# Optimization experiments

Measured on AMD Instinct MI355X. Metric: run time of the kernel, lower is better.

## Reference

```python
import jax, jax.numpy as jnp
import numpy as np

K = 4096       # in_features (reduction dim)
N = 11008      # out_features
GROUP = 128    # scale group size along K
PACK = 8       # int4 values per int32


def dequantize_int4(packed, scales):
    """packed: [K//8, N] int32 (8 int4 nibbles per word along K),
    scales: [K//GROUP, N] fp16. Returns fp16 weight [K, N] with
    w = (nibble - 8) * scale (symmetric zero-point-8 scheme)."""
    shifts = (jnp.arange(PACK, dtype=jnp.int32) * 4)
    # [K//8, 8, N] -> [K, N]
    nibbles = (packed[:, None, :] >> shifts[None, :, None]) & 0xF
    q = nibbles.reshape(K, N)
    s = jnp.repeat(scales, GROUP, axis=0)  # [K, N]
    return (q.astype(jnp.float16) - jnp.float16(8.0)) * s


def setup_inputs() -> dict:
    key = jax.random.key(0)
    k1, k2, k3, k4 = jax.random.split(key, 4)
    x = jax.random.normal(k1, (4, 1024, K), dtype=jnp.float16)
    packed = jax.random.randint(k2, (K // PACK, N), 0, 2147483647, dtype=jnp.int32)
    scales = (jax.random.uniform(k3, (K // GROUP, N), dtype=jnp.float32) * 0.02 + 0.001).astype(jnp.float16)
    bias = jax.random.normal(k4, (N,), dtype=jnp.float16)
    return {"x": x, "packed": packed, "scales": scales, "bias": bias}


def reference(x, packed, scales, bias):
    in_shape = x.shape
    x2 = x.reshape(-1, in_shape[-1]).astype(jnp.float16)  # [M, K]
    w = dequantize_int4(packed, scales)                    # [K, N]
    out = jnp.matmul(x2, w)                                # [M, N] fp16
    out = out.reshape(*in_shape[:-1], -1)
    return out + bias
```

## Files before the change

kernel.cpp:

```cpp
#include <hip/hip_runtime.h>
#include <hip/hip_bf16.h>
#include <stdint.h>

#define K_DIM 4096
#define N_DIM 11008
#define BM 256
#define BN 128
#define NT (K_DIM / 64)

typedef _Float16 half8 __attribute__((ext_vector_type(8)));
typedef _Float16 half2v __attribute__((ext_vector_type(2)));
typedef float floatx4 __attribute__((ext_vector_type(4)));

typedef const uint32_t __attribute__((address_space(1)))* gas_u32p;
typedef uint32_t __attribute__((address_space(3)))* las_u32p;

__device__ __forceinline__ void glds16(const void* g, void* l) {
    __builtin_amdgcn_global_load_lds((gas_u32p)g, (las_u32p)l, 16, 0, 0);
}

__device__ __forceinline__ half8 dequant_word_pk(uint32_t w, half2v s2) {
    const uint32_t M = 0x000F000Fu;
    const uint32_t B = 0x64006400u;
    union { uint32_t u; half2v h; } t0, t1, t2, t3;
    t0.u = (w & M) | B;
    t1.u = ((w >> 4) & M) | B;
    t2.u = ((w >> 8) & M) | B;
    t3.u = ((w >> 12) & M) | B;
    const half2v off = {(_Float16)1032.0f, (_Float16)1032.0f};
    union { half8 h8; half2v h2[4]; } o;
    o.h2[0] = (t0.h - off) * s2;
    o.h2[1] = (t1.h - off) * s2;
    o.h2[2] = (t2.h - off) * s2;
    o.h2[3] = (t3.h - off) * s2;
    return o.h8;
}

__device__ __forceinline__ half8 dequant_word_f16(uint32_t w, float s) {
    half8 r;
    #pragma unroll
    for (int j = 0; j < 8; ++j) {
        int q = (int)((w >> (4 * j)) & 0xFu);
        r[j] = (_Float16)((float)(q - 8) * s);
    }
    return r;
}

__global__ __launch_bounds__(256)
void cvt_kernel(const float* __restrict__ X, _Float16* __restrict__ Xh) {
    size_t idx = (size_t)blockIdx.x * 256 + threadIdx.x;
    size_t base = idx * 8;
    float4 a = *(const float4*)(X + base);
    float4 b = *(const float4*)(X + base + 4);
    half8 h;
    h[0] = (_Float16)a.x; h[1] = (_Float16)b.x;
    h[2] = (_Float16)a.y; h[3] = (_Float16)b.y;
    h[4] = (_Float16)a.z; h[5] = (_Float16)b.z;
    h[6] = (_Float16)a.w; h[7] = (_Float16)b.w;
    *(half8*)(Xh + base) = h;
}

__global__ __launch_bounds__(256, 2)
void qgemm_lds(const _Float16* __restrict__ Xh,
               const int* __restrict__ Wp,
               const float* __restrict__ Sc,
               const float* __restrict__ Bias,
               float* __restrict__ Out)
{
    __shared__ half8 As[BM * 8];

    const int tid = threadIdx.x;
    const int m0 = blockIdx.x * BM;
    const int n0 = blockIdx.y * BN;

    const int lane = tid & 63;
    const int wid  = tid >> 6;
    const int wm   = wid >> 1;
    const int wn   = wid & 1;
    const int q    = lane >> 4;
    const int tt   = lane & 15;

    const int arow = tid >> 3;
    const int ac   = (tid & 7) ^ (arow & 7);
    const _Float16* aSrc = Xh + (size_t)(m0 + arow) * K_DIM + ac * 8;

    const int ncol = n0 + wn * 64 + tt;
    const int* bPtr = Wp + (size_t)q * N_DIM + ncol;
    const float* scPtr = Sc + ncol;

    floatx4 acc[8][4];
    #pragma unroll
    for (int i = 0; i < 8; ++i)
        #pragma unroll
        for (int j = 0; j < 4; ++j)
            acc[i][j] = floatx4{0.f, 0.f, 0.f, 0.f};

    const int x7  = tt & 7;
    const int rb0 = tt * 128 + ((0 * 4 + q) ^ x7) * 16;
    const int rb1 = tt * 128 + ((1 * 4 + q) ^ x7) * 16;
    const char* asBase = (const char*)As + wm * 16384;

    half2v s2[4], sn2[4];
    #pragma unroll
    for (int j = 0; j < 4; ++j) {
        _Float16 sh = (_Float16)scPtr[j * 16];
        s2[j] = (half2v){sh, sh};
    }
    uint32_t wv[8];
    #pragma unroll
    for (int ks = 0; ks < 2; ++ks)
        #pragma unroll
        for (int j = 0; j < 4; ++j)
            wv[ks * 4 + j] = (uint32_t)bPtr[(size_t)(ks * 4) * N_DIM + j * 16];

    for (int kt = 0; kt < NT; ++kt) {
        if (kt > 0 && (kt & 1) == 0) {
            #pragma unroll
            for (int j = 0; j < 4; ++j) s2[j] = sn2[j];
        }

        #pragma unroll
        for (int i = 0; i < 8; ++i)
            glds16(aSrc + (size_t)i * 32 * K_DIM + kt * 64,
                   (char*)As + (size_t)(i * 256 + tid) * 16);

        half8 bf[8];
        #pragma unroll
        for (int ks = 0; ks < 2; ++ks)
            #pragma unroll
            for (int j = 0; j < 4; ++j)
                bf[ks * 4 + j] = dequant_word_pk(wv[ks * 4 + j], s2[j]);

        if (kt + 1 < NT) {
            const int* bp = bPtr + (size_t)(kt + 1) * 8 * N_DIM;
            #pragma unroll
            for (int ks = 0; ks < 2; ++ks)
                #pragma unroll
                for (int j = 0; j < 4; ++j)
                    wv[ks * 4 + j] = (uint32_t)bp[(size_t)(ks * 4) * N_DIM + j * 16];
            if (kt & 1) {
                const float* sp = scPtr + (size_t)((kt + 1) >> 1) * N_DIM;
                #pragma unroll
                for (int j = 0; j < 4; ++j) {
                    _Float16 sh = (_Float16)sp[j * 16];
                    sn2[j] = (half2v){sh, sh};
                }
            }
        }

        __syncthreads();

        #pragma unroll
        for (int ks = 0; ks < 2; ++ks) {
            const int rb = ks ? rb1 : rb0;
            #pragma unroll
            for (int i = 0; i < 8; ++i) {
                half8 af = *(const half8*)(asBase + rb + i * 2048);
                #pragma unroll
                for (int j = 0; j < 4; ++j)
                    acc[i][j] = __builtin_amdgcn_mfma_f32_16x16x32_f16(
                        af, bf[ks * 4 + j], acc[i][j], 0, 0, 0);
            }
        }

        __syncthreads();
    }

    #pragma unroll
    for (int j = 0; j < 4; ++j) {
        const int n = ncol + j * 16;
        const float bv = Bias[n];
        #pragma unroll
        for (int i = 0; i < 8; ++i) {
            const int mrow = m0 + wm * 128 + i * 16 + q * 4;
            #pragma unroll
            for (int r = 0; r < 4; ++r)
                Out[(size_t)(mrow + r) * N_DIM + n] = acc[i][j][r] + bv;
        }
    }
}

__global__ __launch_bounds__(256, 2)
void qgemm_direct(const float* __restrict__ X,
                  const int* __restrict__ Wp,
                  const float* __restrict__ Sc,
                  const float* __restrict__ Bias,
                  float* __restrict__ Out)
{
    const int tid = threadIdx.x;
    const int m0 = blockIdx.x * BM;
    const int n0 = blockIdx.y * BN;
    const int lane = tid & 63;
    const int wid  = tid >> 6;
    const int wm   = wid >> 1;
    const int wn   = wid & 1;
    const int q    = lane >> 4;
    const int tt   = lane & 15;

    const int ncol = n0 + wn * 64 + tt;
    const int* bPtr = Wp + (size_t)q * N_DIM + ncol;
    const float* scPtr = Sc + ncol;
    const float* aBase = X + (size_t)(m0 + wm * 128 + tt) * K_DIM + q * 8;

    floatx4 acc[8][4];
    #pragma unroll
    for (int i = 0; i < 8; ++i)
        #pragma unroll
        for (int j = 0; j < 4; ++j)
            acc[i][j] = floatx4{0.f, 0.f, 0.f, 0.f};

    float s[4];
    for (int kt = 0; kt < NT; ++kt) {
        if ((kt & 1) == 0) {
            const float* sp = scPtr + (size_t)(kt >> 1) * N_DIM;
            #pragma unroll
            for (int j = 0; j < 4; ++j) s[j] = sp[j * 16];
        }
        const int* bp = bPtr + (size_t)kt * 8 * N_DIM;
        uint32_t wv[8];
        #pragma unroll
        for (int ks = 0; ks < 2; ++ks)
            #pragma unroll
            for (int j = 0; j < 4; ++j)
                wv[ks * 4 + j] = (uint32_t)bp[(size_t)(ks * 4) * N_DIM + j * 16];
        half8 bf[8];
        #pragma unroll
        for (int ks = 0; ks < 2; ++ks)
            #pragma unroll
            for (int j = 0; j < 4; ++j)
                bf[ks * 4 + j] = dequant_word_f16(wv[ks * 4 + j], s[j]);
        #pragma unroll
        for (int ks = 0; ks < 2; ++ks) {
            const size_t ko = (size_t)(kt * 64 + ks * 32);
            #pragma unroll
            for (int i = 0; i < 8; ++i) {
                const float* ap = aBase + (size_t)i * 16 * K_DIM + ko;
                float4 lo = *(const float4*)ap;
                float4 hi = *(const float4*)(ap + 4);
                half8 af;
                af[0] = (_Float16)lo.x; af[1] = (_Float16)lo.y;
                af[2] = (_Float16)lo.z; af[3] = (_Float16)lo.w;
                af[4] = (_Float16)hi.x; af[5] = (_Float16)hi.y;
                af[6] = (_Float16)hi.z; af[7] = (_Float16)hi.w;
                #pragma unroll
                for (int j = 0; j < 4; ++j)
                    acc[i][j] = __builtin_amdgcn_mfma_f32_16x16x32_f16(
                        af, bf[ks * 4 + j], acc[i][j], 0, 0, 0);
            }
        }
    }
    #pragma unroll
    for (int j = 0; j < 4; ++j) {
        const int n = ncol + j * 16;
        const float bv = Bias[n];
        #pragma unroll
        for (int i = 0; i < 8; ++i) {
            const int mrow = m0 + wm * 128 + i * 16 + q * 4;
            #pragma unroll
            for (int r = 0; r < 4; ++r)
                Out[(size_t)(mrow + r) * N_DIM + n] = acc[i][j][r] + bv;
        }
    }
}

extern "C" void kernel_launch(void* const* d_in, const int* in_sizes, int n_in,
                              void* d_out, int out_size, void* d_ws, size_t ws_size,
                              hipStream_t stream) {
    (void)in_sizes; (void)n_in; (void)out_size;
    const float* X    = (const float*)d_in[0];
    const int*   Wp   = (const int*)d_in[1];
    const float* Sc   = (const float*)d_in[2];
    const float* Bias = (const float*)d_in[3];
    float*       Out  = (float*)d_out;

    dim3 grid(4096 / BM, N_DIM / BN);
    const size_t needed = (size_t)4096 * K_DIM * sizeof(_Float16);

    if (ws_size >= needed) {
        _Float16* Xh = (_Float16*)d_ws;
        cvt_kernel<<<(4096 * K_DIM) / (256 * 8), 256, 0, stream>>>(X, Xh);
        qgemm_lds<<<grid, 256, 0, stream>>>(Xh, Wp, Sc, Bias, Out);
    } else {
        qgemm_direct<<<grid, 256, 0, stream>>>(X, Wp, Sc, Bias, Out);
    }
}
```

Before: 638.5 us.

## Double-buffer activation tile in LDS with async prefetch of next K-tile

Splits the shared-memory A tile into two buffers. While MFMAs consume the current K-tile, global_load_lds fills the other buffer with the next one, replacing the two per-iteration __syncthreads with a single barrier preceded by a partial vmcnt wait. The goal is to hide global-to-LDS latency behind compute. It doubles LDS use to 64 KB per block, which may limit occupancy, and it depends on hand-counted vmcnt values that must match the number of outstanding weight and scale loads.

```diff
diff --git a/kernel.cpp b/kernel.cpp
--- a/kernel.cpp
+++ b/kernel.cpp
@@ -67,7 +67,7 @@
                const float* __restrict__ Bias,
                float* __restrict__ Out)
 {
-    __shared__ half8 As[BM * 8];
+    __shared__ half8 As[2][BM * 8];
 
     const int tid = threadIdx.x;
     const int m0 = blockIdx.x * BM;
@@ -98,7 +98,12 @@
     const int x7  = tt & 7;
     const int rb0 = tt * 128 + ((0 * 4 + q) ^ x7) * 16;
     const int rb1 = tt * 128 + ((1 * 4 + q) ^ x7) * 16;
-    const char* asBase = (const char*)As + wm * 16384;
+
+    #pragma unroll
+    for (int i = 0; i < 8; ++i)
+        glds16(aSrc + (size_t)i * 32 * K_DIM,
+               (char*)As[0] + (size_t)(i * 256 + tid) * 16);
+    __builtin_amdgcn_sched_barrier(0);
 
     half2v s2[4], sn2[4];
     #pragma unroll
@@ -113,16 +118,25 @@
         for (int j = 0; j < 4; ++j)
             wv[ks * 4 + j] = (uint32_t)bPtr[(size_t)(ks * 4) * N_DIM + j * 16];
 
+    asm volatile("s_waitcnt vmcnt(0)" ::: "memory");
+    __builtin_amdgcn_s_barrier();
+    __builtin_amdgcn_sched_barrier(0);
+
     for (int kt = 0; kt < NT; ++kt) {
+        const int cur = kt & 1;
+
         if (kt > 0 && (kt & 1) == 0) {
             #pragma unroll
             for (int j = 0; j < 4; ++j) s2[j] = sn2[j];
         }
 
-        #pragma unroll
-        for (int i = 0; i < 8; ++i)
-            glds16(aSrc + (size_t)i * 32 * K_DIM + kt * 64,
-                   (char*)As + (size_t)(i * 256 + tid) * 16);
+        if (kt + 1 < NT) {
+            #pragma unroll
+            for (int i = 0; i < 8; ++i)
+                glds16(aSrc + (size_t)i * 32 * K_DIM + (kt + 1) * 64,
+                       (char*)As[cur ^ 1] + (size_t)(i * 256 + tid) * 16);
+        }
+        __builtin_amdgcn_sched_barrier(0);
 
         half8 bf[8];
         #pragma unroll
@@ -148,14 +162,13 @@
             }
         }
 
-        __syncthreads();
-
+        const char* ab = (const char*)As[cur] + wm * 16384;
         #pragma unroll
         for (int ks = 0; ks < 2; ++ks) {
             const int rb = ks ? rb1 : rb0;
             #pragma unroll
             for (int i = 0; i < 8; ++i) {
-                half8 af = *(const half8*)(asBase + rb + i * 2048);
+                half8 af = *(const half8*)(ab + rb + i * 2048);
                 #pragma unroll
                 for (int j = 0; j < 4; ++j)
                     acc[i][j] = __builtin_amdgcn_mfma_f32_16x16x32_f16(
@@ -163,7 +176,12 @@
             }
         }
 
-        __syncthreads();
+        if (kt + 1 < NT) {
+            if (kt & 1) { asm volatile("s_waitcnt vmcnt(12)" ::: "memory"); }
+            else        { asm volatile("s_waitcnt vmcnt(8)"  ::: "memory"); }
+            __builtin_amdgcn_s_barrier();
+            __builtin_amdgcn_sched_barrier(0);
+        }
     }
 
     #pragma unroll
```

Measured after the change: 613.0 us. 4.0% less time.
